# Kernel optimization log

Hardware: AMD Instinct MI355X
Metric: run time of the kernel (lower is better)

## Reference

```python
import jax, jax.numpy as jnp
import numpy as np

D_MODEL = 1024
N_HEADS = 16
D_HEAD = D_MODEL // N_HEADS
D_FF = 4096
EPS = 1e-5


def layernorm(x, gamma, beta):
    mu = jnp.mean(x, axis=-1, keepdims=True)
    var = jnp.var(x, axis=-1, keepdims=True)
    return (x - mu) * jax.lax.rsqrt(var + EPS) * gamma + beta


def setup_inputs() -> dict:
    key = jax.random.key(0)
    ks = jax.random.split(key, 16)
    B, T = 4, 2048
    s = 1.0 / np.sqrt(D_MODEL)
    sf = 1.0 / np.sqrt(D_FF)
    return {
        "x": jax.random.normal(ks[0], (B, T, D_MODEL), jnp.float32),
        "gate_score": jax.random.uniform(ks[1], (B,), jnp.float32),
        "Wq": jax.random.normal(ks[2], (D_MODEL, D_MODEL), jnp.float32) * s,
        "bq": jnp.zeros((D_MODEL,), jnp.float32),
        "Wk": jax.random.normal(ks[3], (D_MODEL, D_MODEL), jnp.float32) * s,
        "bk": jnp.zeros((D_MODEL,), jnp.float32),
        "Wv": jax.random.normal(ks[4], (D_MODEL, D_MODEL), jnp.float32) * s,
        "bv": jnp.zeros((D_MODEL,), jnp.float32),
        "Wo": jax.random.normal(ks[5], (D_MODEL, D_MODEL), jnp.float32) * s,
        "bo": jnp.zeros((D_MODEL,), jnp.float32),
        "W1": jax.random.normal(ks[6], (D_MODEL, D_FF), jnp.float32) * s,
        "b1": jnp.zeros((D_FF,), jnp.float32),
        "W2": jax.random.normal(ks[7], (D_FF, D_MODEL), jnp.float32) * sf,
        "b2": jnp.zeros((D_MODEL,), jnp.float32),
        "gamma1": jnp.ones((D_MODEL,), jnp.float32),
        "beta1": jnp.zeros((D_MODEL,), jnp.float32),
        "gamma2": jnp.ones((D_MODEL,), jnp.float32),
        "beta2": jnp.zeros((D_MODEL,), jnp.float32),
    }


def reference(x, gate_score, Wq, bq, Wk, bk, Wv, bv, Wo, bo,
              W1, b1, W2, b2, gamma1, beta1, gamma2, beta2):
    B, T, C = x.shape
    # --- attention sub-block (pre-norm) ---
    h = layernorm(x, gamma1, beta1)
    Q = (h @ Wq + bq).reshape(B, T, N_HEADS, D_HEAD).transpose(0, 2, 1, 3)
    K = (h @ Wk + bk).reshape(B, T, N_HEADS, D_HEAD).transpose(0, 2, 1, 3)
    V = (h @ Wv + bv).reshape(B, T, N_HEADS, D_HEAD).transpose(0, 2, 1, 3)
    scores = jnp.einsum("bhqd,bhkd->bhqk", Q, K) / np.sqrt(D_HEAD)
    causal = jnp.tril(jnp.ones((T, T), dtype=bool))  # True = keep
    scores = jnp.where(causal, scores, -jnp.inf)
    attn = jax.nn.softmax(scores, axis=-1)
    ctx = jnp.einsum("bhqk,bhkd->bhqd", attn, V)
    ctx = ctx.transpose(0, 2, 1, 3).reshape(B, T, C)
    attn_out = ctx @ Wo + bo
    x1 = x + attn_out
    # --- FFN sub-block (pre-norm) ---
    h2 = layernorm(x1, gamma2, beta2)
    ff = jax.nn.gelu(h2 @ W1 + b1, approximate=False) @ W2 + b2
    x2 = x1 + ff
    # --- gated residual ---
    g = gate_score[:, None, None]
    return x + g * (x2 - x)
```

## Files before the change

### kernel.cpp

```cpp
#include <hip/hip_runtime.h>
#include <hip/hip_bf16.h>
#include <cmath>

typedef unsigned short u16;
typedef __attribute__((ext_vector_type(8))) short short8;
typedef __attribute__((ext_vector_type(4))) float f32x4;

#define DM 1024
#define NH 16
#define DH 64
#define DFF 4096
#define BB 4
#define TT 2048
#define MROWS (BB*TT)

__device__ __forceinline__ float bu2f(u16 u) {
    union { float f; unsigned v; } c; c.v = ((unsigned)u) << 16; return c.f;
}
__device__ __forceinline__ u16 f2bu(float f) {
    __hip_bfloat16 h = __float2bfloat16(f);
    union { __hip_bfloat16 h; u16 u; } c; c.h = h; return c.u;
}
__device__ __forceinline__ void async_copy16(const u16* g, u16* l) {
    __builtin_amdgcn_global_load_lds((const __attribute__((address_space(1))) void*)g,
                                     (__attribute__((address_space(3))) void*)l, 16, 0, 0);
}

__global__ void ln_kernel(const float* __restrict__ x, const float* __restrict__ gamma,
                          const float* __restrict__ beta, u16* __restrict__ out)
{
    int row = blockIdx.x;
    int tid = threadIdx.x;
    float4 v4 = ((const float4*)(x + (size_t)row * DM))[tid];
    float v[4] = { v4.x, v4.y, v4.z, v4.w };
    float s = v[0] + v[1] + v[2] + v[3];
    float ss = v[0]*v[0] + v[1]*v[1] + v[2]*v[2] + v[3]*v[3];
    #pragma unroll
    for (int o = 32; o > 0; o >>= 1) { s += __shfl_down(s, o); ss += __shfl_down(ss, o); }
    __shared__ float red[8];
    int w = tid >> 6;
    if ((tid & 63) == 0) { red[w] = s; red[4 + w] = ss; }
    __syncthreads();
    s  = red[0] + red[1] + red[2] + red[3];
    ss = red[4] + red[5] + red[6] + red[7];
    float mu  = s * (1.0f / DM);
    float var = ss * (1.0f / DM) - mu * mu;
    float rstd = rsqrtf(var + 1e-5f);
    float4 g4 = ((const float4*)gamma)[tid];
    float4 b4 = ((const float4*)beta)[tid];
    float g[4] = { g4.x, g4.y, g4.z, g4.w };
    float b[4] = { b4.x, b4.y, b4.z, b4.w };
    ushort4 o4;
    u16* op = (u16*)&o4;
    #pragma unroll
    for (int i = 0; i < 4; i++) op[i] = f2bu((v[i] - mu) * rstd * g[i] + b[i]);
    ((ushort4*)(out + (size_t)row * DM))[tid] = o4;
}

__global__ void transpose4_f2b(const float* __restrict__ w0, const float* __restrict__ w1,
                               const float* __restrict__ w2, const float* __restrict__ w3,
                               u16* __restrict__ outQKV, u16* __restrict__ outO)
{
    __shared__ u16 tile[32][33];
    const float* in = (blockIdx.z == 0) ? w0 : (blockIdx.z == 1) ? w1
                     : (blockIdx.z == 2) ? w2 : w3;
    u16* out = (blockIdx.z < 3) ? (outQKV + (size_t)blockIdx.z * DM * DM) : outO;
    int bx = blockIdx.x * 32;
    int by = blockIdx.y * 32;
    int tx = threadIdx.x, ty = threadIdx.y;
    #pragma unroll
    for (int i = 0; i < 32; i += 8)
        tile[ty + i][tx] = f2bu(in[(size_t)(by + ty + i) * DM + bx + tx]);
    __syncthreads();
    #pragma unroll
    for (int i = 0; i < 32; i += 8)
        out[(size_t)(bx + ty + i) * DM + by + tx] = tile[tx][ty + i];
}

__global__ void transpose_f2b(const float* __restrict__ in, u16* __restrict__ out,
                              int R, int C)
{
    __shared__ u16 tile[32][33];
    int bx = blockIdx.x * 32;
    int by = blockIdx.y * 32;
    int tx = threadIdx.x, ty = threadIdx.y;
    #pragma unroll
    for (int i = 0; i < 32; i += 8)
        tile[ty + i][tx] = f2bu(in[(size_t)(by + ty + i) * C + bx + tx]);
    __syncthreads();
    #pragma unroll
    for (int i = 0; i < 32; i += 8)
        out[(size_t)(bx + ty + i) * R + by + tx] = tile[tx][ty + i];
}

#define BM 128
#define BN 128
#define BK 64

template<int EPI>
__global__ void gemm_bt(
    const u16* __restrict__ A, const u16* __restrict__ Bt,
    const float* __restrict__ bias, const float* __restrict__ bias2,
    const float* __restrict__ bias3, void* __restrict__ Cv,
    const float* __restrict__ res, const float* __restrict__ x0,
    const float* __restrict__ gate, int M, int N, int K)
{
    __shared__ __align__(16) u16 As[BM * BK];
    __shared__ __align__(16) u16 Bs[BN * BK];
    int tid = threadIdx.x;
    int lane = tid & 63, wave = tid >> 6;
    int wm = (wave & 1) * 64, wn = (wave >> 1) * 64;
    int lm = lane & 15, quad = lane >> 4;
    size_t row0 = (size_t)blockIdx.x * BM;
    size_t col0 = (size_t)blockIdx.y * BN;

    int sr = tid >> 3;
    int scol = (((tid & 7) ^ (sr & 7)) * 8);
    const u16* Ag = A  + (row0 + sr) * (size_t)K + scol;
    const u16* Bg = Bt + (col0 + sr) * (size_t)K + scol;
    u16* Asl = As + tid * 8;
    u16* Bsl = Bs + tid * 8;

    int fc0 = ((0 * 4 + quad) ^ (lm & 7)) * 8;
    int fc1 = ((1 * 4 + quad) ^ (lm & 7)) * 8;

    f32x4 acc[4][4];
    #pragma unroll
    for (int i = 0; i < 4; i++)
        #pragma unroll
        for (int j = 0; j < 4; j++)
            acc[i][j] = (f32x4){0.f, 0.f, 0.f, 0.f};

    for (int k0 = 0; k0 < K; k0 += BK) {
        __syncthreads();
        async_copy16(Ag + k0,                  Asl);
        async_copy16(Ag + (size_t)32 * K + k0, Asl + 32 * BK);
        async_copy16(Ag + (size_t)64 * K + k0, Asl + 64 * BK);
        async_copy16(Ag + (size_t)96 * K + k0, Asl + 96 * BK);
        async_copy16(Bg + k0,                  Bsl);
        async_copy16(Bg + (size_t)32 * K + k0, Bsl + 32 * BK);
        async_copy16(Bg + (size_t)64 * K + k0, Bsl + 64 * BK);
        async_copy16(Bg + (size_t)96 * K + k0, Bsl + 96 * BK);
        __syncthreads();
        #pragma unroll
        for (int ks = 0; ks < 2; ks++) {
            int fc = ks ? fc1 : fc0;
            short8 af[4], bfr[4];
            #pragma unroll
            for (int t = 0; t < 4; t++) {
                af[t]  = *(const short8*)&As[(wm + t * 16 + lm) * BK + fc];
                bfr[t] = *(const short8*)&Bs[(wn + t * 16 + lm) * BK + fc];
            }
            #pragma unroll
            for (int mt = 0; mt < 4; mt++)
                #pragma unroll
                for (int nt = 0; nt < 4; nt++)
                    acc[mt][nt] = __builtin_amdgcn_mfma_f32_16x16x32_bf16(
                        af[mt], bfr[nt], acc[mt][nt], 0, 0, 0);
        }
    }

    u16*   C16 = (u16*)Cv;
    float* Cf  = (float*)Cv;

    const float* bb = bias;
    size_t csub = 0;
    if (EPI == 0 && bias2 != nullptr) {
        size_t cbase = col0 + wn;
        if (cbase >= 2048)      { bb = bias3; csub = 2048; }
        else if (cbase >= 1024) { bb = bias2; csub = 1024; }
    }

    #pragma unroll
    for (int mt = 0; mt < 4; mt++) {
        #pragma unroll
        for (int nt = 0; nt < 4; nt++) {
            #pragma unroll
            for (int r = 0; r < 4; r++) {
                size_t row = row0 + wm + mt * 16 + quad * 4 + r;
                size_t col = col0 + wn + nt * 16 + lm;
                size_t idx = row * (size_t)N + col;
                float v = acc[mt][nt][r] + bb[col - csub];
                if (EPI == 0) {
                    C16[idx] = f2bu(v);
                } else if (EPI == 1) {
                    Cf[idx] = v + res[idx];
                } else if (EPI == 2) {
                    v = 0.5f * v * (1.0f + erff(v * 0.70710678118f));
                    C16[idx] = f2bu(v);
                } else {
                    float xv  = x0[idx];
                    float x1v = res[idx];
                    float g   = gate[row >> 11];
                    Cf[idx] = xv + g * (x1v + v - xv);
                }
            }
        }
    }
}

#define AVS 72

#define TILE_STEP(O, L, A0, A1, QW, QV, KB) do {                                   \
    f32x4 s_[4];                                                                   \
    _Pragma("unroll")                                                              \
    for (int ks = 0; ks < 4; ks++) s_[ks] = (f32x4){0.f, 0.f, 0.f, 0.f};           \
    _Pragma("unroll")                                                              \
    for (int ks = 0; ks < 4; ks++) {                                               \
        short8 k0_ = *(const short8*)&Kl[ks * 16 + lm][quad * 8];                  \
        short8 k1_ = *(const short8*)&Kl[ks * 16 + lm][32 + quad * 8];             \
        s_[ks] = __builtin_amdgcn_mfma_f32_16x16x32_bf16(k0_, (A0), s_[ks], 0, 0, 0); \
        s_[ks] = __builtin_amdgcn_mfma_f32_16x16x32_bf16(k1_, (A1), s_[ks], 0, 0, 0); \
    }                                                                              \
    bool mz_ = ((KB) + 63 > (QW));                                                 \
    _Pragma("unroll")                                                              \
    for (int ks = 0; ks < 4; ks++) {                                               \
        int kbase_ = (KB) + ks * 16 + quad * 4;                                    \
        ushort4 pk_;                                                               \
        u16* pp_ = (u16*)&pk_;                                                     \
        _Pragma("unroll")                                                          \
        for (int r = 0; r < 4; r++) {                                              \
            float v_ = s_[ks][r] * sc - FM;                                        \
            if (mz_ && (kbase_ + r > (QV))) v_ = -INFINITY;                        \
            pp_[r] = f2bu(exp2f(v_));                                              \
        }                                                                          \
        *(ushort4*)&Pl[w][lm][ks * 16 + quad * 4] = pk_;                           \
    }                                                                              \
    _Pragma("unroll")                                                              \
    for (int kc = 0; kc < 2; kc++) {                                               \
        short8 ap_ = *(const short8*)&Pl[w][lm][kc * 32 + quad * 8];               \
        _Pragma("unroll")                                                          \
        for (int ds = 0; ds < 4; ds++) {                                           \
            short8 bv_ = *(const short8*)&Vt[ds * 16 + lm][kc * 32 + quad * 8];    \
            O[ds] = __builtin_amdgcn_mfma_f32_16x16x32_bf16(ap_, bv_, O[ds], 0, 0, 0); \
        }                                                                          \
        L = __builtin_amdgcn_mfma_f32_16x16x32_bf16(ap_, ones, L, 0, 0, 0);        \
    }                                                                              \
} while (0)

__global__ __launch_bounds__(256, 4) void attn_mfma(
    const u16* __restrict__ QKV, u16* __restrict__ ctx)
{
    __shared__ __align__(16) u16 Kl[64][AVS];
    __shared__ __align__(16) u16 Vt[64][AVS];
    __shared__ __align__(16) u16 Pl[4][16][AVS];

    const int LD = 3 * DM;
    int tid = threadIdx.x, lane = tid & 63, w = tid >> 6;
    int lm = lane & 15, quad = lane >> 4;

    int bi = blockIdx.x;
    int pair = bi & 15, h = (bi >> 4) & 15, b = bi >> 8;
    int t1 = 31 - pair, t2 = pair;

    const size_t hoff = (size_t)h * DH;
    const u16* Qp = QKV + (size_t)b * TT * LD + hoff;
    const u16* Kp = Qp + DM;
    const u16* Vp = Qp + 2 * DM;

    int qw1 = t1 * 64 + w * 16, qv1 = qw1 + lm;
    int qw2 = t2 * 64 + w * 16, qv2 = qw2 + lm;

    short8 aq1_0 = *(const short8*)(Qp + (size_t)(qw1 + lm) * LD + quad * 8);
    short8 aq1_1 = *(const short8*)(Qp + (size_t)(qw1 + lm) * LD + 32 + quad * 8);
    short8 aq2_0 = *(const short8*)(Qp + (size_t)(qw2 + lm) * LD + quad * 8);
    short8 aq2_1 = *(const short8*)(Qp + (size_t)(qw2 + lm) * LD + 32 + quad * 8);

    int kkey = tid & 63, kdim = (tid >> 6) * 16;
    int vkey = (tid & 31) * 2, vdim = (tid >> 5) * 8;

    const u16* kb0 = Kp + (size_t)kkey * LD + kdim;
    const u16* vb0 = Vp + (size_t)vkey * LD + vdim;
    const u16* vb1 = Vp + (size_t)(vkey + 1) * LD + vdim;

    const float sc = 0.18033688011f;
    const float FM = 24.0f;
    const short s1 = (short)0x3F80;
    const short8 ones = (short8){s1, s1, s1, s1, s1, s1, s1, s1};

    f32x4 o1[4], o2[4], l1, l2;
    #pragma unroll
    for (int ds = 0; ds < 4; ds++) {
        o1[ds] = (f32x4){0.f, 0.f, 0.f, 0.f};
        o2[ds] = (f32x4){0.f, 0.f, 0.f, 0.f};
    }
    l1 = (f32x4){0.f, 0.f, 0.f, 0.f};
    l2 = (f32x4){0.f, 0.f, 0.f, 0.f};

    uint4 kr0 = *(const uint4*)(kb0);
    uint4 kr1 = *(const uint4*)(kb0 + 8);
    uint4 vr0 = *(const uint4*)(vb0);
    uint4 vr1 = *(const uint4*)(vb1);

    int nch = t1 + 1;
    for (int c = 0; c < nch; c++) {
        int kb = c * 64;
        __syncthreads();
        *(uint4*)&Kl[kkey][kdim]     = kr0;
        *(uint4*)&Kl[kkey][kdim + 8] = kr1;
        {
            const u16* p0 = (const u16*)&vr0;
            const u16* p1 = (const u16*)&vr1;
            #pragma unroll
            for (int j = 0; j < 8; j++) {
                ushort2 pk = { p0[j], p1[j] };
                *(ushort2*)&Vt[vdim + j][vkey] = pk;
            }
        }
        __syncthreads();

        {
            size_t offn = (c + 1 < nch) ? (size_t)(c + 1) * 64 * LD : 0;
            kr0 = *(const uint4*)(kb0 + offn);
            kr1 = *(const uint4*)(kb0 + offn + 8);
            vr0 = *(const uint4*)(vb0 + offn);
            vr1 = *(const uint4*)(vb1 + offn);
        }

        TILE_STEP(o1, l1, aq1_0, aq1_1, qw1, qv1, kb);
        if (c <= t2)
            TILE_STEP(o2, l2, aq2_0, aq2_1, qw2, qv2, kb);
    }

    {
        float inv[4];
        #pragma unroll
        for (int r = 0; r < 4; r++) inv[r] = 1.0f / l1[r];
        #pragma unroll
        for (int ds = 0; ds < 4; ds++)
            #pragma unroll
            for (int r = 0; r < 4; r++) {
                size_t row = (size_t)(b * TT + qw1 + quad * 4 + r);
                ctx[row * DM + hoff + ds * 16 + lm] = f2bu(o1[ds][r] * inv[r]);
            }
        #pragma unroll
        for (int r = 0; r < 4; r++) inv[r] = 1.0f / l2[r];
        #pragma unroll
        for (int ds = 0; ds < 4; ds++)
            #pragma unroll
            for (int r = 0; r < 4; r++) {
                size_t row = (size_t)(b * TT + qw2 + quad * 4 + r);
                ctx[row * DM + hoff + ds * 16 + lm] = f2bu(o2[ds][r] * inv[r]);
            }
    }
}

extern "C" void kernel_launch(void* const* d_in, const int* in_sizes, int n_in,
                              void* d_out, int out_size, void* d_ws, size_t ws_size,
                              hipStream_t stream)
{
    const float* x    = (const float*)d_in[0];
    const float* gate = (const float*)d_in[1];
    const float* Wq   = (const float*)d_in[2];
    const float* bq   = (const float*)d_in[3];
    const float* Wk   = (const float*)d_in[4];
    const float* bk   = (const float*)d_in[5];
    const float* Wv   = (const float*)d_in[6];
    const float* bv   = (const float*)d_in[7];
    const float* Wo   = (const float*)d_in[8];
    const float* bo   = (const float*)d_in[9];
    const float* W1   = (const float*)d_in[10];
    const float* b1   = (const float*)d_in[11];
    const float* W2   = (const float*)d_in[12];
    const float* b2   = (const float*)d_in[13];
    const float* gamma1 = (const float*)d_in[14];
    const float* beta1  = (const float*)d_in[15];
    const float* gamma2 = (const float*)d_in[16];
    const float* beta2  = (const float*)d_in[17];
    float* out = (float*)d_out;

    char* ws = (char*)d_ws;
    const size_t MB = 1024 * 1024;
    u16* WtQKV = (u16*)(ws + 0 * MB);
    u16* WtO   = (u16*)(ws + 6 * MB);
    u16* Wt1   = (u16*)(ws + 8 * MB);
    u16* Wt2   = (u16*)(ws + 16 * MB);
    u16* h     = (u16*)(ws + 24 * MB);
    u16* ctx   = (u16*)(ws + 24 * MB);
    u16* QKVb  = (u16*)(ws + 40 * MB);
    float* x1  = (float*)(ws + 40 * MB);
    u16* h2    = (u16*)(ws + 72 * MB);
    u16* ff    = (u16*)(ws + 88 * MB);

    dim3 tb(32, 8);
    transpose4_f2b<<<dim3(32, 32, 4), tb, 0, stream>>>(Wq, Wk, Wv, Wo, WtQKV, WtO);
    transpose_f2b<<<dim3(DFF / 32, DM / 32), tb, 0, stream>>>(W1, Wt1, DM, DFF);
    transpose_f2b<<<dim3(DM / 32, DFF / 32), tb, 0, stream>>>(W2, Wt2, DFF, DM);

    ln_kernel<<<MROWS, 256, 0, stream>>>(x, gamma1, beta1, h);

    gemm_bt<0><<<dim3(MROWS / BM, 3 * DM / BN), 256, 0, stream>>>(
        h, WtQKV, bq, bk, bv, QKVb, nullptr, nullptr, nullptr, MROWS, 3 * DM, DM);

    attn_mfma<<<BB * NH * 16, 256, 0, stream>>>(QKVb, ctx);

    gemm_bt<1><<<dim3(MROWS / BM, DM / BN), 256, 0, stream>>>(
        ctx, WtO, bo, nullptr, nullptr, x1, x, nullptr, nullptr, MROWS, DM, DM);

    ln_kernel<<<MROWS, 256, 0, stream>>>(x1, gamma2, beta2, h2);

    gemm_bt<2><<<dim3(MROWS / BM, DFF / BN), 256, 0, stream>>>(
        h2, Wt1, b1, nullptr, nullptr, ff, nullptr, nullptr, nullptr, MROWS, DFF, DM);

    gemm_bt<3><<<dim3(MROWS / BM, DM / BN), 256, 0, stream>>>(
        ff, Wt2, b2, nullptr, nullptr, out, x1, x, gate, MROWS, DM, DFF);
}
```

Measured before the change: 547.0 us.

## Swizzle attention LDS layout, split causal mask path, and remap workgroups across XCDs

The attention kernel's K, V-transpose and P tiles in LDS switch from padded rows to XOR-swizzled 64-wide rows. This cuts LDS use and is meant to avoid bank conflicts. The softmax exponent step now has a separate unmasked fast path using fmaf, so the per-element mask check only runs on diagonal tiles. Both the GEMM and attention kernels remap block indices so consecutive logical tiles are spread across the 8 XCDs, improving L2 locality. The risks are swizzle index mistakes and extra index arithmetic.

After: 560.2 us. 1.02x slower.

```diff
diff --git a/kernel.cpp b/kernel.cpp
--- a/kernel.cpp
+++ b/kernel.cpp
@@ -111,8 +111,15 @@
     int lane = tid & 63, wave = tid >> 6;
     int wm = (wave & 1) * 64, wn = (wave >> 1) * 64;
     int lm = lane & 15, quad = lane >> 4;
-    size_t row0 = (size_t)blockIdx.x * BM;
-    size_t col0 = (size_t)blockIdx.y * BN;
+
+    unsigned nbx = gridDim.x;
+    unsigned nwg = nbx * gridDim.y;
+    unsigned orig = blockIdx.y * nbx + blockIdx.x;
+    unsigned swz = (orig & 7) * (nwg >> 3) + (orig >> 3);
+    unsigned bxi = swz % nbx, byi = swz / nbx;
+
+    size_t row0 = (size_t)bxi * BM;
+    size_t col0 = (size_t)byi * BN;
 
     int sr = tid >> 3;
     int scol = (((tid & 7) ^ (sr & 7)) * 8);
@@ -199,7 +206,7 @@
     }
 }
 
-#define AVS 72
+#define SW8(row, c8) ((((c8) ^ ((row) & 7)) * 8))
 
 #define TILE_STEP(O, L, A0, A1, QW, QV, KB) do {                                   \
     f32x4 s_[4];                                                                   \
@@ -207,31 +214,44 @@
     for (int ks = 0; ks < 4; ks++) s_[ks] = (f32x4){0.f, 0.f, 0.f, 0.f};           \
     _Pragma("unroll")                                                              \
     for (int ks = 0; ks < 4; ks++) {                                               \
-        short8 k0_ = *(const short8*)&Kl[ks * 16 + lm][quad * 8];                  \
-        short8 k1_ = *(const short8*)&Kl[ks * 16 + lm][32 + quad * 8];             \
+        int kr_ = ks * 16 + lm;                                                    \
+        short8 k0_ = *(const short8*)&Kl[kr_][SW8(lm, quad)];                      \
+        short8 k1_ = *(const short8*)&Kl[kr_][SW8(lm, 4 + quad)];                  \
         s_[ks] = __builtin_amdgcn_mfma_f32_16x16x32_bf16(k0_, (A0), s_[ks], 0, 0, 0); \
         s_[ks] = __builtin_amdgcn_mfma_f32_16x16x32_bf16(k1_, (A1), s_[ks], 0, 0, 0); \
     }                                                                              \
     bool mz_ = ((KB) + 63 > (QW));                                                 \
-    _Pragma("unroll")                                                              \
-    for (int ks = 0; ks < 4; ks++) {                                               \
-        int kbase_ = (KB) + ks * 16 + quad * 4;                                    \
-        ushort4 pk_;                                                               \
-        u16* pp_ = (u16*)&pk_;                                                     \
+    if (!mz_) {                                                                    \
         _Pragma("unroll")                                                          \
-        for (int r = 0; r < 4; r++) {                                              \
-            float v_ = s_[ks][r] * sc - FM;                                        \
-            if (mz_ && (kbase_ + r > (QV))) v_ = -INFINITY;                        \
-            pp_[r] = f2bu(exp2f(v_));                                              \
+        for (int ks = 0; ks < 4; ks++) {                                           \
+            ushort4 pk_;                                                           \
+            u16* pp_ = (u16*)&pk_;                                                 \
+            _Pragma("unroll")                                                      \
+            for (int r = 0; r < 4; r++)                                            \
+                pp_[r] = f2bu(exp2f(fmaf(s_[ks][r], sc, -FM)));                    \
+            *(ushort4*)&Pl[w][lm][SW8(lm, ks * 2 + (quad >> 1)) + (quad & 1) * 4] = pk_; \
         }                                                                          \
-        *(ushort4*)&Pl[w][lm][ks * 16 + quad * 4] = pk_;                           \
+    } else {                                                                       \
+        _Pragma("unroll")                                                          \
+        for (int ks = 0; ks < 4; ks++) {                                           \
+            int kbase_ = (KB) + ks * 16 + quad * 4;                                \
+            ushort4 pk_;                                                           \
+            u16* pp_ = (u16*)&pk_;                                                 \
+            _Pragma("unroll")                                                      \
+            for (int r = 0; r < 4; r++) {                                          \
+                float v_ = fmaf(s_[ks][r], sc, -FM);                               \
+                if (kbase_ + r > (QV)) v_ = -INFINITY;                             \
+                pp_[r] = f2bu(exp2f(v_));                                          \
+            }                                                                      \
+            *(ushort4*)&Pl[w][lm][SW8(lm, ks * 2 + (quad >> 1)) + (quad & 1) * 4] = pk_; \
+        }                                                                          \
     }                                                                              \
     _Pragma("unroll")                                                              \
     for (int kc = 0; kc < 2; kc++) {                                               \
-        short8 ap_ = *(const short8*)&Pl[w][lm][kc * 32 + quad * 8];               \
+        short8 ap_ = *(const short8*)&Pl[w][lm][SW8(lm, kc * 4 + quad)];           \
         _Pragma("unroll")                                                          \
         for (int ds = 0; ds < 4; ds++) {                                           \
-            short8 bv_ = *(const short8*)&Vt[ds * 16 + lm][kc * 32 + quad * 8];    \
+            short8 bv_ = *(const short8*)&Vt[ds * 16 + lm][SW8(lm, kc * 4 + quad)]; \
             O[ds] = __builtin_amdgcn_mfma_f32_16x16x32_bf16(ap_, bv_, O[ds], 0, 0, 0); \
         }                                                                          \
         L = __builtin_amdgcn_mfma_f32_16x16x32_bf16(ap_, ones, L, 0, 0, 0);        \
@@ -241,15 +261,16 @@
 __global__ __launch_bounds__(256, 4) void attn_mfma(
     const u16* __restrict__ QKV, u16* __restrict__ ctx)
 {
-    __shared__ __align__(16) u16 Kl[64][AVS];
-    __shared__ __align__(16) u16 Vt[64][AVS];
-    __shared__ __align__(16) u16 Pl[4][16][AVS];
+    __shared__ __align__(16) u16 Kl[64][64];
+    __shared__ __align__(16) u16 Vt[64][64];
+    __shared__ __align__(16) u16 Pl[4][16][64];
 
     const int LD = 3 * DM;
     int tid = threadIdx.x, lane = tid & 63, w = tid >> 6;
     int lm = lane & 15, quad = lane >> 4;
 
-    int bi = blockIdx.x;
+    unsigned orig = blockIdx.x;
+    int bi = (int)((orig & 7) * 128 + (orig >> 3));
     int pair = bi & 15, h = (bi >> 4) & 15, b = bi >> 8;
     int t1 = 31 - pair, t2 = pair;
 
@@ -292,19 +313,23 @@
     uint4 vr0 = *(const uint4*)(vb0);
     uint4 vr1 = *(const uint4*)(vb1);
 
+    int ksw0 = SW8(kkey, (tid >> 6) * 2);
+    int ksw1 = SW8(kkey, (tid >> 6) * 2 + 1);
+    int vc8 = vkey >> 3, vlo = vkey & 7;
+
     int nch = t1 + 1;
     for (int c = 0; c < nch; c++) {
         int kb = c * 64;
         __syncthreads();
-        *(uint4*)&Kl[kkey][kdim]     = kr0;
-        *(uint4*)&Kl[kkey][kdim + 8] = kr1;
+        *(uint4*)&Kl[kkey][ksw0] = kr0;
+        *(uint4*)&Kl[kkey][ksw1] = kr1;
         {
             const u16* p0 = (const u16*)&vr0;
             const u16* p1 = (const u16*)&vr1;
             #pragma unroll
             for (int j = 0; j < 8; j++) {
                 ushort2 pk = { p0[j], p1[j] };
-                *(ushort2*)&Vt[vdim + j][vkey] = pk;
+                *(ushort2*)&Vt[vdim + j][((vc8 ^ j) * 8) + vlo] = pk;
             }
         }
         __syncthreads();
```
